# Kernel optimization log

Measured on AMD Instinct MI355X. Metric: run time of the kernel, lower is better.

Reference implementation:

```python
import jax, jax.numpy as jnp
import numpy as np


def setup_inputs() -> dict:
    key = jax.random.key(0)
    k1, k2 = jax.random.split(key)
    x = jax.random.normal(k1, (4, 4096, 1024), dtype=jnp.float32)
    codebook = jax.random.normal(k2, (16384, 1024), dtype=jnp.float32)
    return {"x": x, "codebook": codebook}


def reference(x, codebook):
    # Euclidean snap: argmin over pairwise L2 distances, then gather.
    # Squared distances suffice for argmin (monotone transform of cdist p=2).
    x2 = jnp.sum(x * x, axis=-1, keepdims=True)            # [b, n, 1]
    c2 = jnp.sum(codebook * codebook, axis=-1)             # [c]
    xc = jnp.einsum('bnd,cd->bnc', x, codebook)            # [b, n, c]
    d2 = x2 - 2.0 * xc + c2                                # [b, n, c]
    codebook_ids = jnp.argmin(d2, axis=-1)                 # [b, n]
    output = jnp.take(codebook, codebook_ids, axis=0)      # [b, n, d]
    return output
```

## Files before the change

kernel.cpp:

```cpp
#include <hip/hip_runtime.h>
#include <hip/hip_bf16.h>
#include <hip/hip_fp8.h>
#include <stdint.h>

#define NROWS  16384
#define NCODES 16384
#define DIM    1024
#define NT     16
#define MARGIN_Q 514

typedef float f32x4  __attribute__((ext_vector_type(4)));
typedef short bf16x8 __attribute__((ext_vector_type(8)));
typedef long  longx2 __attribute__((ext_vector_type(2)));
typedef unsigned char uchar;

__device__ __forceinline__ ushort f2bf(float f) {
  uint32_t u = __float_as_uint(f);
  uint32_t r = u + 0x7FFFu + ((u >> 16) & 1u);
  return (ushort)(r >> 16);
}
__device__ __forceinline__ int imin(int a, int b){ return a < b ? a : b; }
__device__ __forceinline__ int imax(int a, int b){ return a < b ? b : a; }
__device__ __forceinline__ int packKey32(float s, int idx) {
  int q = (int)rintf(s * 16.0f);
  return q * 16384 + idx;
}

#define GLDS16(gp, lp) \
  __builtin_amdgcn_global_load_lds((const __attribute__((address_space(1))) void*)(gp), \
                                   (__attribute__((address_space(3))) void*)(lp), 16, 0, 0)

__device__ __forceinline__ void sbar() {
  asm volatile("" ::: "memory");
  __builtin_amdgcn_s_barrier();
  asm volatile("" ::: "memory");
}

__global__ __launch_bounds__(256) void c2_kernel(const float* __restrict__ cb,
                                                 float* __restrict__ c2) {
  const int code = blockIdx.x;
  const int t = threadIdx.x, lane = t & 63, wid = t >> 6;
  f32x4 v = *(const f32x4*)(cb + (size_t)code * DIM + t * 4);
  float s = v[0]*v[0] + v[1]*v[1] + v[2]*v[2] + v[3]*v[3];
  #pragma unroll
  for (int off = 32; off; off >>= 1) s += __shfl_down(s, off);
  __shared__ float part[4];
  if (lane == 0) part[wid] = s;
  __syncthreads();
  if (t == 0) c2[code] = part[0] + part[1] + part[2] + part[3];
}

__global__ __launch_bounds__(256) void convert_fp8_pair(const float* __restrict__ src,
                                                        uchar* __restrict__ dst) {
  const int chunk = blockIdx.x * 256 + threadIdx.x;
  const int p   = chunk & 3;
  const int row = (chunk >> 2) & 255;
  const int kt  = (chunk >> 10) & 15;
  const int m   = chunk >> 14;
  const int q   = p ^ ((row >> 1) & 3);
  const float* s = src + (size_t)(m * 256 + row) * DIM + kt * 64 + q * 8;
  uint64_t lo = 0, hi = 0;
  #pragma unroll
  for (int j = 0; j < 8; ++j) {
    __hip_fp8_e4m3 a(s[j]);
    __hip_fp8_e4m3 b(s[j + 32]);
    lo |= (uint64_t)a.__x << (8 * j);
    hi |= (uint64_t)b.__x << (8 * j);
  }
  uint64_t* o = (uint64_t*)(dst + (size_t)chunk * 16);
  o[0] = lo; o[1] = hi;
}


#define STAGE_A(BUF, KT) do {                                                     \
    GLDS16(ga + (KT)*16384,        &lsA[BUF][w*1024]);                            \
    GLDS16(ga + (KT)*16384 + 8192, &lsA[BUF][w*1024 + 8192]);                     \
  } while (0)
#define STAGE_B(BUF, KT) do {                                                     \
    GLDS16(gb + (KT)*16384,        &lsB[BUF][w*1024]);                            \
    GLDS16(gb + (KT)*16384 + 8192, &lsB[BUF][w*1024 + 8192]);                     \
  } while (0)

#define RD_A(MIB, BUF) do {                                                       \
    _Pragma("unroll")                                                             \
    for (int mi_ = 0; mi_ < 4; ++mi_) {                                           \
      longx2 v_ = *(const longx2*)(Apos[BUF] + ((MIB) + mi_) * 1024);             \
      aF[mi_][0] = v_[0]; aF[mi_][1] = v_[1];                                     \
    } } while (0)
#define RD_B(BUF) do {                                                            \
    _Pragma("unroll")                                                             \
    for (int ni_ = 0; ni_ < 4; ++ni_) {                                           \
      longx2 v_ = *(const longx2*)(Bpos[BUF] + ni_ * 1024);                       \
      bF[ni_][0] = v_[0]; bF[ni_][1] = v_[1];                                     \
    } } while (0)

#define MMA_Q(MB, NB) do {                                                        \
    __builtin_amdgcn_s_setprio(1);                                                \
    _Pragma("unroll")                                                             \
    for (int ks_ = 0; ks_ < 2; ++ks_) {                                           \
      _Pragma("unroll")                                                           \
      for (int mi_ = 0; mi_ < 4; ++mi_) {                                         \
        _Pragma("unroll")                                                         \
        for (int ni_ = 0; ni_ < 2; ++ni_)                                         \
          acc[(MB) + mi_][(NB) + ni_] = __builtin_amdgcn_mfma_f32_16x16x32_fp8_fp8( \
              aF[mi_][ks_], bF[(NB) + ni_][ks_], acc[(MB) + mi_][(NB) + ni_], 0, 0, 0); \
      } }                                                                         \
    __builtin_amdgcn_s_setprio(0);                                                \
  } while (0)

#define G0  asm volatile("s_waitcnt vmcnt(0)" ::: "memory")
#define NOG do {} while (0)

#define TILE(KT, CUR, NXT, DOST, GUARD) do {                                      \
    if (DOST) { STAGE_A(NXT, (KT) + 1); STAGE_B(NXT, (KT) + 1); }                 \
    RD_B(CUR);                                                                    \
    RD_A(0, CUR);                                                                 \
    MMA_Q(0, 0); MMA_Q(0, 2);                                                     \
    RD_A(4, CUR);                                                                 \
    MMA_Q(4, 0); MMA_Q(4, 2);                                                     \
    asm volatile("s_waitcnt lgkmcnt(0)" ::: "memory");                            \
    GUARD;                                                                        \
    sbar();                                                                       \
  } while (0)

__global__ __launch_bounds__(512, 2) void snap_gemm256(const uchar* __restrict__ xs,
                                                       const uchar* __restrict__ cs,
                                                       const float* __restrict__ c2,
                                                       int* __restrict__ cand) {
  __shared__ uchar lsA[2][16384];
  __shared__ uchar lsB[2][16384];

  const int t    = threadIdx.x;
  const int lane = t & 63;
  const int w    = t >> 6;
  const int wm   = w >> 2;
  const int wn   = w & 3;
  const int l15  = lane & 15;
  const int kgrp = lane >> 4;

  const int bid = blockIdx.x;
  const int swz = (bid & 7) * 512 + (bid >> 3);
  const int bm  = swz & 63;
  const int bn  = swz >> 6;

  const uchar* ga = xs + (size_t)bm * 16 * 16384 + w * 1024 + lane * 16;
  const uchar* gb = cs + (size_t)bn * 16 * 16384 + w * 1024 + lane * 16;

  const int posoff = (kgrp ^ ((l15 >> 1) & 3)) * 16;
  const int arow   = (wm * 128 + l15) * 64;
  const int brow   = (wn * 64  + l15) * 64;
  const uchar* Apos[2]; const uchar* Bpos[2];
  #pragma unroll
  for (int b = 0; b < 2; ++b) { Apos[b] = &lsA[b][arow + posoff]; Bpos[b] = &lsB[b][brow + posoff]; }

  f32x4 acc[8][4];
  #pragma unroll
  for (int mi = 0; mi < 8; ++mi)
    #pragma unroll
    for (int ni = 0; ni < 4; ++ni)
      acc[mi][ni] = (f32x4){0.f, 0.f, 0.f, 0.f};

  long aF[4][2], bF[4][2];

  STAGE_A(0, 0); STAGE_B(0, 0);
  G0;
  sbar();

  TILE(0 , 0, 1, 1, G0);
  TILE(1 , 1, 0, 1, G0);
  TILE(2 , 0, 1, 1, G0);
  TILE(3 , 1, 0, 1, G0);
  TILE(4 , 0, 1, 1, G0);
  TILE(5 , 1, 0, 1, G0);
  TILE(6 , 0, 1, 1, G0);
  TILE(7 , 1, 0, 1, G0);
  TILE(8 , 0, 1, 1, G0);
  TILE(9 , 1, 0, 1, G0);
  TILE(10, 0, 1, 1, G0);
  TILE(11, 1, 0, 1, G0);
  TILE(12, 0, 1, 1, G0);
  TILE(13, 1, 0, 1, G0);
  TILE(14, 0, 1, 1, G0);
  TILE(15, 1, 0, 0, NOG);

  __syncthreads();

  int* red = (int*)&lsA[0][0];
  float c2v[4];
  int   colv[4];
  #pragma unroll
  for (int ni = 0; ni < 4; ++ni) {
    colv[ni] = bn * 256 + wn * 64 + ni * 16 + l15;
    c2v[ni]  = c2[colv[ni]];
  }

  #pragma unroll
  for (int mi = 0; mi < 8; ++mi) {
    #pragma unroll
    for (int r = 0; r < 4; ++r) {
      int a = packKey32(fmaf(-2.0f, acc[mi][0][r], c2v[0]), colv[0]);
      int b = packKey32(fmaf(-2.0f, acc[mi][1][r], c2v[1]), colv[1]);
      int c = packKey32(fmaf(-2.0f, acc[mi][2][r], c2v[2]), colv[2]);
      int d = packKey32(fmaf(-2.0f, acc[mi][3][r], c2v[3]), colv[3]);
      int lo1 = imin(a, b), hi1 = imax(a, b);
      int lo2 = imin(c, d), hi2 = imax(c, d);
      int k1 = imin(lo1, lo2);
      int k2 = imin(imax(lo1, lo2), imin(hi1, hi2));
      #pragma unroll
      for (int m = 1; m < 16; m <<= 1) {
        int o1 = __shfl_xor(k1, m);
        int o2 = __shfl_xor(k2, m);
        int n1 = imin(k1, o1);
        int n2 = imin(imax(k1, o1), imin(k2, o2));
        k1 = n1; k2 = n2;
      }
      if (l15 == 0) {
        int rl = wm * 128 + mi * 16 + kgrp * 4 + r;
        red[(wn * 256 + rl) * 2 + 0] = k1;
        red[(wn * 256 + rl) * 2 + 1] = k2;
      }
    }
  }
  __syncthreads();

  if (t < 256) {
    int k1 = red[(0 * 256 + t) * 2 + 0];
    int k2 = red[(0 * 256 + t) * 2 + 1];
    #pragma unroll
    for (int q = 1; q < 4; ++q) {
      int p1 = red[(q * 256 + t) * 2 + 0];
      int p2 = red[(q * 256 + t) * 2 + 1];
      int n1 = imin(k1, p1);
      int n2 = imin(imax(k1, p1), imin(k2, p2));
      k1 = n1; k2 = n2;
    }
    size_t o = (size_t)(bm * 256 + t) * 128 + (size_t)bn * 2;
    cand[o]     = k1;
    cand[o + 1] = k2;
  }
}

__global__ __launch_bounds__(256) void snap_gemm_slow(const float* __restrict__ x,
                                                      const float* __restrict__ cb,
                                                      const float* __restrict__ c2,
                                                      int* __restrict__ cand) {
  __shared__ ushort lsA[2][8192];
  __shared__ ushort lsB[2][8192];
  __shared__ int redbuf[2][128][2];

  const int t    = threadIdx.x;
  const int lane = t & 63;
  const int wid  = t >> 6;
  const int wm   = wid & 1;
  const int wn   = wid >> 1;
  const int l15  = lane & 15;
  const int kgrp = lane >> 4;

  const int bm = blockIdx.x & 127;
  const int bn = blockIdx.x >> 7;
  const int rowBase = bm * 128;
  const int colBase = bn * 128;

  const float* aptr[4];
  const float* bptr[4];
  int ldsOff[4];
  #pragma unroll
  for (int i = 0; i < 4; ++i) {
    int pc = t + 256 * i;
    int row = pc >> 3;
    int g = (pc & 7) ^ (row & 7);
    aptr[i] = x  + (size_t)(rowBase + row) * DIM + g * 8;
    bptr[i] = cb + (size_t)(colBase + row) * DIM + g * 8;
    ldsOff[i] = pc * 8;
  }

  f32x4 acc[4][4];
  #pragma unroll
  for (int mi = 0; mi < 4; ++mi)
    #pragma unroll
    for (int ni = 0; ni < 4; ++ni)
      acc[mi][ni] = (f32x4){0.f, 0.f, 0.f, 0.f};

  auto STAGE = [&](int buf, int kt) {
    const int kOff = kt * 64;
    #pragma unroll
    for (int i = 0; i < 4; ++i) {
      f32x4 a0 = *(const f32x4*)(aptr[i] + kOff);
      f32x4 a1 = *(const f32x4*)(aptr[i] + kOff + 4);
      f32x4 b0 = *(const f32x4*)(bptr[i] + kOff);
      f32x4 b1 = *(const f32x4*)(bptr[i] + kOff + 4);
      bf16x8 pa, pb;
      #pragma unroll
      for (int j = 0; j < 4; ++j) {
        pa[j]     = (short)f2bf(a0[j]);
        pa[j + 4] = (short)f2bf(a1[j]);
        pb[j]     = (short)f2bf(b0[j]);
        pb[j + 4] = (short)f2bf(b1[j]);
      }
      *(bf16x8*)(&lsA[buf][ldsOff[i]]) = pa;
      *(bf16x8*)(&lsB[buf][ldsOff[i]]) = pb;
    }
  };

  STAGE(0, 0);
  __syncthreads();

  for (int kt = 0; kt < DIM / 64; ++kt) {
    const int cur = kt & 1;
    if (kt < DIM / 64 - 1) STAGE(cur ^ 1, kt + 1);

    const ushort* bA = &lsA[cur][0];
    const ushort* bB = &lsB[cur][0];
    #pragma unroll
    for (int ks = 0; ks < 2; ++ks) {
      const int gidx = ks * 4 + kgrp;
      bf16x8 af[4], bfr[4];
      #pragma unroll
      for (int mi = 0; mi < 4; ++mi) {
        int r_ = wm * 64 + mi * 16 + l15;
        af[mi] = *(const bf16x8*)(bA + (r_ * 8 + (gidx ^ (r_ & 7))) * 8);
      }
      #pragma unroll
      for (int ni = 0; ni < 4; ++ni) {
        int c_ = wn * 64 + ni * 16 + l15;
        bfr[ni] = *(const bf16x8*)(bB + (c_ * 8 + (gidx ^ (c_ & 7))) * 8);
      }
      #pragma unroll
      for (int mi = 0; mi < 4; ++mi)
        #pragma unroll
        for (int ni = 0; ni < 4; ++ni)
          acc[mi][ni] = __builtin_amdgcn_mfma_f32_16x16x32_bf16(af[mi], bfr[ni], acc[mi][ni], 0, 0, 0);
    }
    __syncthreads();
  }

  float c2v[4];
  int   colv[4];
  #pragma unroll
  for (int ni = 0; ni < 4; ++ni) {
    colv[ni] = colBase + wn * 64 + ni * 16 + l15;
    c2v[ni]  = c2[colv[ni]];
  }

  #pragma unroll
  for (int mi = 0; mi < 4; ++mi) {
    #pragma unroll
    for (int r = 0; r < 4; ++r) {
      int a = packKey32(fmaf(-2.0f, acc[mi][0][r], c2v[0]), colv[0]);
      int b = packKey32(fmaf(-2.0f, acc[mi][1][r], c2v[1]), colv[1]);
      int c = packKey32(fmaf(-2.0f, acc[mi][2][r], c2v[2]), colv[2]);
      int d = packKey32(fmaf(-2.0f, acc[mi][3][r], c2v[3]), colv[3]);
      int lo1 = imin(a, b), hi1 = imax(a, b);
      int lo2 = imin(c, d), hi2 = imax(c, d);
      int k1 = imin(lo1, lo2);
      int k2 = imin(imax(lo1, lo2), imin(hi1, hi2));
      #pragma unroll
      for (int m = 1; m < 16; m <<= 1) {
        int o1 = __shfl_xor(k1, m);
        int o2 = __shfl_xor(k2, m);
        int n1 = imin(k1, o1);
        int n2 = imin(imax(k1, o1), imin(k2, o2));
        k1 = n1; k2 = n2;
      }
      if (l15 == 0) {
        int rl = wm * 64 + mi * 16 + kgrp * 4 + r;
        redbuf[wn][rl][0] = k1;
        redbuf[wn][rl][1] = k2;
      }
    }
  }
  __syncthreads();

  if (t < 128) {
    int a1 = redbuf[0][t][0], a2 = redbuf[0][t][1];
    int b1 = redbuf[1][t][0], b2 = redbuf[1][t][1];
    int m1 = imin(a1, b1);
    int m2 = imin(imax(a1, b1), imin(a2, b2));
    size_t o = (size_t)(rowBase + t) * 256 + (size_t)bn * 2;
    cand[o]     = m1;
    cand[o + 1] = m2;
  }
}

__global__ __launch_bounds__(256) void rerank(const float* __restrict__ x,
                                              const float* __restrict__ cb,
                                              const int* __restrict__ cand,
                                              int* __restrict__ bestidx,
                                              int poolN) {
  const int row = blockIdx.x;
  const int t = threadIdx.x, lane = t & 63, wid = t >> 6;
  __shared__ int    smin[4];
  __shared__ int    gshared;
  __shared__ double dpart[4];
  __shared__ int    cnt;
  __shared__ int    list[64];

  int my = (t < poolN) ? cand[(size_t)row * poolN + t] : 0x7FFFFFFF;
  int k = my;
  #pragma unroll
  for (int off = 32; off; off >>= 1) k = imin(k, __shfl_down(k, off));
  if (lane == 0) smin[wid] = k;
  if (t == 0) cnt = 0;
  __syncthreads();
  if (t == 0) {
    int g = smin[0];
    for (int i = 1; i < 4; ++i) g = imin(g, smin[i]);
    gshared = g;
  }
  __syncthreads();

  const int gq = gshared >> 14;
  if ((my >> 14) <= gq + MARGIN_Q) {
    int p = atomicAdd(&cnt, 1);
    if (p < 64) list[p] = my & 16383;
  }
  __syncthreads();
  int n = cnt; if (n > 64) n = 64;

  uint64_t best = ~0ull;
  const float* xr = x + (size_t)row * DIM;
  for (int i = 0; i < n; ++i) {
    const int cidx = list[i];
    const float* cr = cb + (size_t)cidx * DIM;
    double p = 0.0;
    #pragma unroll
    for (int j = 0; j < 4; ++j) {
      int d = t + 256 * j;
      double diff = (double)xr[d] - (double)cr[d];
      p += diff * diff;
    }
    #pragma unroll
    for (int off = 32; off; off >>= 1) p += __shfl_down(p, off);
    if (lane == 0) dpart[wid] = p;
    __syncthreads();
    if (t == 0) {
      double d2 = dpart[0] + dpart[1] + dpart[2] + dpart[3];
      uint64_t bits = (uint64_t)__double_as_longlong(d2);
      uint64_t key = (bits & ~0x3FFFull) | (uint32_t)cidx;
      if (key < best) best = key;
    }
    __syncthreads();
  }
  if (t == 0) bestidx[row] = (int)(best & 0x3FFFull);
}

__global__ __launch_bounds__(256) void gather_rows(const float* __restrict__ cb,
                                                   const int* __restrict__ bestidx,
                                                   float* __restrict__ out) {
  const int row = blockIdx.x;
  const int idx = bestidx[row];
  f32x4 v = *(const f32x4*)(cb + (size_t)idx * DIM + threadIdx.x * 4);
  *(f32x4*)(out + (size_t)row * DIM + threadIdx.x * 4) = v;
}

extern "C" void kernel_launch(void* const* d_in, const int* in_sizes, int n_in,
                              void* d_out, int out_size, void* d_ws, size_t ws_size,
                              hipStream_t stream) {
  const float* x  = (const float*)d_in[0];
  const float* cb = (const float*)d_in[1];
  float* out = (float*)d_out;

  float* c2      = (float*)d_ws;
  int*   bestidx = (int*)((char*)d_ws + 64 * 1024);

  const size_t candBytes = (size_t)NROWS * 128 * 4;
  const size_t needFast  = 128 * 1024 + candBytes;

  c2_kernel<<<NCODES, 256, 0, stream>>>(cb, c2);

  if (ws_size >= needFast) {
    uchar* xs = (uchar*)d_out;
    uchar* cs = xs + (size_t)NROWS * DIM;
    int* cand = (int*)((char*)d_ws + 128 * 1024);

    convert_fp8_pair<<<4096, 256, 0, stream>>>(x,  xs);
    convert_fp8_pair<<<4096, 256, 0, stream>>>(cb, cs);
    snap_gemm256<<<4096, 512, 0, stream>>>(xs, cs, c2, cand);
    rerank<<<NROWS, 256, 0, stream>>>(x, cb, cand, bestidx, 128);
    gather_rows<<<NROWS, 256, 0, stream>>>(cb, bestidx, out);
  } else {
    int* cand = (int*)d_out;
    snap_gemm_slow<<<(NROWS / 128) * (NCODES / 128), 256, 0, stream>>>(x, cb, c2, cand);
    rerank<<<NROWS, 256, 0, stream>>>(x, cb, cand, bestidx, 256);
    gather_rows<<<NROWS, 256, 0, stream>>>(cb, bestidx, out);
  }
}
```

Measured before the change: 591.9 us.

## Switch FP8 GEMM to 32x32x64 scaled MFMA with matching operand layout

Replaces the 16x16x32 fp8 MFMA inner loop with the gfx950 mfma_scale_f32_32x32x64_f8f6f4 instruction, using unit scales (0x7F exponent). The conversion kernel is rewritten to emit a new fp8 LDS layout that matches the 32x32x64 operand fragments. The LDS reads, accumulator shapes and epilogue top-2 reduction are remapped to the 32-lane output layout. The aim is fewer MFMA issues and higher matrix throughput per tile. The risk is more register pressure from the 16-wide accumulators and possible LDS bank conflicts, since the old XOR swizzle is removed.

```diff
diff --git a/kernel.cpp b/kernel.cpp
--- a/kernel.cpp
+++ b/kernel.cpp
@@ -9,9 +9,11 @@
 #define NT     16
 #define MARGIN_Q 514
 
-typedef float f32x4  __attribute__((ext_vector_type(4)));
-typedef short bf16x8 __attribute__((ext_vector_type(8)));
-typedef long  longx2 __attribute__((ext_vector_type(2)));
+typedef float f32x4   __attribute__((ext_vector_type(4)));
+typedef float f32x16  __attribute__((ext_vector_type(16)));
+typedef int   i32x4   __attribute__((ext_vector_type(4)));
+typedef int   i32x8   __attribute__((ext_vector_type(8)));
+typedef short bf16x8  __attribute__((ext_vector_type(8)));
 typedef unsigned char uchar;
 
 __device__ __forceinline__ ushort f2bf(float f) {
@@ -50,27 +52,29 @@
   if (t == 0) c2[code] = part[0] + part[1] + part[2] + part[3];
 }
 
-__global__ __launch_bounds__(256) void convert_fp8_pair(const float* __restrict__ src,
-                                                        uchar* __restrict__ dst) {
-  const int chunk = blockIdx.x * 256 + threadIdx.x;
-  const int p   = chunk & 3;
-  const int row = (chunk >> 2) & 255;
-  const int kt  = (chunk >> 10) & 15;
-  const int m   = chunk >> 14;
-  const int q   = p ^ ((row >> 1) & 3);
-  const float* s = src + (size_t)(m * 256 + row) * DIM + kt * 64 + q * 8;
+__global__ __launch_bounds__(256) void convert_fp8_mx(const float* __restrict__ src,
+                                                      uchar* __restrict__ dst) {
+  const int c  = blockIdx.x * 256 + threadIdx.x;
+  const int wch = c & 1023;
+  const int st = wch >> 7;
+  const int h  = (wch >> 6) & 1;
+  const int l  = wch & 63;
+  const int kt = (c >> 10) & 15;
+  const int m  = c >> 14;
+  const int row = st * 32 + (l & 31);
+  const int kb  = (l >> 5) * 32 + h * 16;
+  const float* s = src + (size_t)(m * 256 + row) * DIM + kt * 64 + kb;
   uint64_t lo = 0, hi = 0;
   #pragma unroll
   for (int j = 0; j < 8; ++j) {
     __hip_fp8_e4m3 a(s[j]);
-    __hip_fp8_e4m3 b(s[j + 32]);
+    __hip_fp8_e4m3 b(s[j + 8]);
     lo |= (uint64_t)a.__x << (8 * j);
     hi |= (uint64_t)b.__x << (8 * j);
   }
-  uint64_t* o = (uint64_t*)(dst + (size_t)chunk * 16);
+  uint64_t* o = (uint64_t*)(dst + (size_t)c * 16);
   o[0] = lo; o[1] = hi;
 }
-
 
 #define STAGE_A(BUF, KT) do {                                                     \
     GLDS16(ga + (KT)*16384,        &lsA[BUF][w*1024]);                            \
@@ -81,30 +85,33 @@
     GLDS16(gb + (KT)*16384 + 8192, &lsB[BUF][w*1024 + 8192]);                     \
   } while (0)
 
-#define RD_A(MIB, BUF) do {                                                       \
+#define RD_A(BUF) do {                                                            \
     _Pragma("unroll")                                                             \
     for (int mi_ = 0; mi_ < 4; ++mi_) {                                           \
-      longx2 v_ = *(const longx2*)(Apos[BUF] + ((MIB) + mi_) * 1024);             \
-      aF[mi_][0] = v_[0]; aF[mi_][1] = v_[1];                                     \
+      i32x4 lo_ = *(const i32x4*)(Abase[BUF] + mi_ * 2048);                       \
+      i32x4 hi_ = *(const i32x4*)(Abase[BUF] + mi_ * 2048 + 1024);                \
+      _Pragma("unroll")                                                           \
+      for (int j_ = 0; j_ < 4; ++j_) { aF[mi_][j_] = lo_[j_]; aF[mi_][4+j_] = hi_[j_]; } \
     } } while (0)
 #define RD_B(BUF) do {                                                            \
     _Pragma("unroll")                                                             \
-    for (int ni_ = 0; ni_ < 4; ++ni_) {                                           \
-      longx2 v_ = *(const longx2*)(Bpos[BUF] + ni_ * 1024);                       \
-      bF[ni_][0] = v_[0]; bF[ni_][1] = v_[1];                                     \
+    for (int nb_ = 0; nb_ < 2; ++nb_) {                                           \
+      i32x4 lo_ = *(const i32x4*)(Bbase[BUF] + nb_ * 2048);                       \
+      i32x4 hi_ = *(const i32x4*)(Bbase[BUF] + nb_ * 2048 + 1024);                \
+      _Pragma("unroll")                                                           \
+      for (int j_ = 0; j_ < 4; ++j_) { bF[nb_][j_] = lo_[j_]; bF[nb_][4+j_] = hi_[j_]; } \
     } } while (0)
 
-#define MMA_Q(MB, NB) do {                                                        \
+#define MMA_ALL do {                                                              \
     __builtin_amdgcn_s_setprio(1);                                                \
     _Pragma("unroll")                                                             \
-    for (int ks_ = 0; ks_ < 2; ++ks_) {                                           \
+    for (int mi_ = 0; mi_ < 4; ++mi_) {                                           \
       _Pragma("unroll")                                                           \
-      for (int mi_ = 0; mi_ < 4; ++mi_) {                                         \
-        _Pragma("unroll")                                                         \
-        for (int ni_ = 0; ni_ < 2; ++ni_)                                         \
-          acc[(MB) + mi_][(NB) + ni_] = __builtin_amdgcn_mfma_f32_16x16x32_fp8_fp8( \
-              aF[mi_][ks_], bF[(NB) + ni_][ks_], acc[(MB) + mi_][(NB) + ni_], 0, 0, 0); \
-      } }                                                                         \
+      for (int nb_ = 0; nb_ < 2; ++nb_)                                           \
+        acc[mi_][nb_] = __builtin_amdgcn_mfma_scale_f32_32x32x64_f8f6f4(          \
+            aF[mi_], bF[nb_], acc[mi_][nb_], 0, 0,                                \
+            0, 0x7F7F7F7F, 0, 0x7F7F7F7F);                                        \
+    }                                                                             \
     __builtin_amdgcn_s_setprio(0);                                                \
   } while (0)
 
@@ -114,10 +121,8 @@
 #define TILE(KT, CUR, NXT, DOST, GUARD) do {                                      \
     if (DOST) { STAGE_A(NXT, (KT) + 1); STAGE_B(NXT, (KT) + 1); }                 \
     RD_B(CUR);                                                                    \
-    RD_A(0, CUR);                                                                 \
-    MMA_Q(0, 0); MMA_Q(0, 2);                                                     \
-    RD_A(4, CUR);                                                                 \
-    MMA_Q(4, 0); MMA_Q(4, 2);                                                     \
+    RD_A(CUR);                                                                    \
+    MMA_ALL;                                                                      \
     asm volatile("s_waitcnt lgkmcnt(0)" ::: "memory");                            \
     GUARD;                                                                        \
     sbar();                                                                       \
@@ -135,8 +140,6 @@
   const int w    = t >> 6;
   const int wm   = w >> 2;
   const int wn   = w & 3;
-  const int l15  = lane & 15;
-  const int kgrp = lane >> 4;
 
   const int bid = blockIdx.x;
   const int swz = (bid & 7) * 512 + (bid >> 3);
@@ -146,21 +149,23 @@
   const uchar* ga = xs + (size_t)bm * 16 * 16384 + w * 1024 + lane * 16;
   const uchar* gb = cs + (size_t)bn * 16 * 16384 + w * 1024 + lane * 16;
 
-  const int posoff = (kgrp ^ ((l15 >> 1) & 3)) * 16;
-  const int arow   = (wm * 128 + l15) * 64;
-  const int brow   = (wn * 64  + l15) * 64;
-  const uchar* Apos[2]; const uchar* Bpos[2];
-  #pragma unroll
-  for (int b = 0; b < 2; ++b) { Apos[b] = &lsA[b][arow + posoff]; Bpos[b] = &lsB[b][brow + posoff]; }
-
-  f32x4 acc[8][4];
-  #pragma unroll
-  for (int mi = 0; mi < 8; ++mi)
-    #pragma unroll
-    for (int ni = 0; ni < 4; ++ni)
-      acc[mi][ni] = (f32x4){0.f, 0.f, 0.f, 0.f};
-
-  long aF[4][2], bF[4][2];
+  const uchar* Abase[2]; const uchar* Bbase[2];
+  #pragma unroll
+  for (int b = 0; b < 2; ++b) {
+    Abase[b] = &lsA[b][wm * 8192 + lane * 16];
+    Bbase[b] = &lsB[b][wn * 4096 + lane * 16];
+  }
+
+  f32x16 acc[4][2];
+  #pragma unroll
+  for (int mi = 0; mi < 4; ++mi)
+    #pragma unroll
+    for (int nb = 0; nb < 2; ++nb)
+      #pragma unroll
+      for (int r = 0; r < 16; ++r)
+        acc[mi][nb][r] = 0.f;
+
+  i32x8 aF[4], bF[2];
 
   STAGE_A(0, 0); STAGE_B(0, 0);
   G0;
@@ -186,38 +191,30 @@
   __syncthreads();
 
   int* red = (int*)&lsA[0][0];
-  float c2v[4];
-  int   colv[4];
-  #pragma unroll
-  for (int ni = 0; ni < 4; ++ni) {
-    colv[ni] = bn * 256 + wn * 64 + ni * 16 + l15;
-    c2v[ni]  = c2[colv[ni]];
-  }
-
-  #pragma unroll
-  for (int mi = 0; mi < 8; ++mi) {
-    #pragma unroll
-    for (int r = 0; r < 4; ++r) {
-      int a = packKey32(fmaf(-2.0f, acc[mi][0][r], c2v[0]), colv[0]);
-      int b = packKey32(fmaf(-2.0f, acc[mi][1][r], c2v[1]), colv[1]);
-      int c = packKey32(fmaf(-2.0f, acc[mi][2][r], c2v[2]), colv[2]);
-      int d = packKey32(fmaf(-2.0f, acc[mi][3][r], c2v[3]), colv[3]);
-      int lo1 = imin(a, b), hi1 = imax(a, b);
-      int lo2 = imin(c, d), hi2 = imax(c, d);
-      int k1 = imin(lo1, lo2);
-      int k2 = imin(imax(lo1, lo2), imin(hi1, hi2));
-      #pragma unroll
-      for (int m = 1; m < 16; m <<= 1) {
+  const int colb = bn * 256 + wn * 64 + (lane & 31);
+  const float c2v0 = c2[colb];
+  const float c2v1 = c2[colb + 32];
+  const int rbase = wm * 128 + 4 * (lane >> 5);
+
+  #pragma unroll
+  for (int mi = 0; mi < 4; ++mi) {
+    #pragma unroll
+    for (int reg = 0; reg < 16; ++reg) {
+      int ka = packKey32(fmaf(-2.0f, acc[mi][0][reg], c2v0), colb);
+      int kb = packKey32(fmaf(-2.0f, acc[mi][1][reg], c2v1), colb + 32);
+      int k1 = imin(ka, kb), k2 = imax(ka, kb);
+      #pragma unroll
+      for (int m = 1; m < 32; m <<= 1) {
         int o1 = __shfl_xor(k1, m);
         int o2 = __shfl_xor(k2, m);
         int n1 = imin(k1, o1);
         int n2 = imin(imax(k1, o1), imin(k2, o2));
         k1 = n1; k2 = n2;
       }
-      if (l15 == 0) {
-        int rl = wm * 128 + mi * 16 + kgrp * 4 + r;
-        red[(wn * 256 + rl) * 2 + 0] = k1;
-        red[(wn * 256 + rl) * 2 + 1] = k2;
+      if ((lane & 31) == 0) {
+        int row = rbase + mi * 32 + (reg & 3) + 8 * (reg >> 2);
+        red[(wn * 256 + row) * 2 + 0] = k1;
+        red[(wn * 256 + row) * 2 + 1] = k2;
       }
     }
   }
@@ -473,8 +470,8 @@
     uchar* cs = xs + (size_t)NROWS * DIM;
     int* cand = (int*)((char*)d_ws + 128 * 1024);
 
-    convert_fp8_pair<<<4096, 256, 0, stream>>>(x,  xs);
-    convert_fp8_pair<<<4096, 256, 0, stream>>>(cb, cs);
+    convert_fp8_mx<<<4096, 256, 0, stream>>>(x,  xs);
+    convert_fp8_mx<<<4096, 256, 0, stream>>>(cb, cs);
     snap_gemm256<<<4096, 512, 0, stream>>>(xs, cs, c2, cand);
     rerank<<<NROWS, 256, 0, stream>>>(x, cb, cand, bestidx, 128);
     gather_rows<<<NROWS, 256, 0, stream>>>(cb, bestidx, out);
```

After: 2.304 ms. 289% more time.
